# Kernel optimization log

Hardware: AMD Instinct MI355X
Metric: run time of the kernel (lower is better)

Reference implementation:

```python
import jax, jax.numpy as jnp
import numpy as np

B, N, T, D, H = 4, 8, 512, 256, 8
DK = D // H


def _dwconv(x, w, b=None):
    # x: (BN, D, T) depthwise conv, kernel 3, padding 'same', groups=D
    y = jax.lax.conv_general_dilated(
        x, w, window_strides=(1,), padding='SAME',
        feature_group_count=x.shape[1],
        dimension_numbers=('NCH', 'OIH', 'NCH'))
    if b is not None:
        y = y + b[None, :, None]
    return y


def setup_inputs() -> dict:
    key = jax.random.key(0)
    ks = jax.random.split(key, 16)
    s = 1.0 / np.sqrt(D)
    s3 = 1.0 / np.sqrt(3 * D)
    inp = {
        'query': jax.random.normal(ks[0], (B, N, T, D), jnp.float32),
        'key': jax.random.normal(ks[1], (B, N, T, D), jnp.float32),
        'value': jax.random.normal(ks[2], (B, N, T, D), jnp.float32),
        'key_padding_mask': jax.random.randint(ks[3], (B, N, T), 0, 2, jnp.int32),
        # depthwise conv params
        'w_pos': jax.random.uniform(ks[4], (D, 1, 3), jnp.float32, -0.577, 0.577),
        'b_pos': jax.random.uniform(ks[5], (D,), jnp.float32, -0.577, 0.577),
        # physics-initialized differential operators (still learnable floats)
        'w_vel': jnp.tile(jnp.array([-1.0, 0.0, 1.0], jnp.float32)[None, None, :], (D, 1, 1)),
        'w_acc': jnp.tile(jnp.array([1.0, -2.0, 1.0], jnp.float32)[None, None, :], (D, 1, 1)),
        # fusion / projection linears (stored as (in, out))
        'Wq': jax.random.uniform(ks[6], (3 * D, D), jnp.float32, -s3, s3),
        'bq': jax.random.uniform(ks[7], (D,), jnp.float32, -s3, s3),
        'Wk': jax.random.uniform(ks[8], (3 * D, D), jnp.float32, -s3, s3),
        'bk': jax.random.uniform(ks[9], (D,), jnp.float32, -s3, s3),
        'Wv': jax.random.uniform(ks[10], (D, D), jnp.float32, -s, s),
        'bv': jax.random.uniform(ks[11], (D,), jnp.float32, -s, s),
        'Wo': jax.random.uniform(ks[12], (D, D), jnp.float32, -s, s),
        'bo': jax.random.uniform(ks[13], (D,), jnp.float32, -s, s),
    }
    return inp


def reference(query, key, value, key_padding_mask,
              w_pos, b_pos, w_vel, w_acc,
              Wq, bq, Wk, bk, Wv, bv, Wo, bo):
    b, n, t, d = query.shape
    scale = jnp.float32(1.0 / np.sqrt(DK))

    def kin_feats(x):
        xin = x.reshape(b * n, t, d).transpose(0, 2, 1)  # (BN, D, T)
        p = _dwconv(xin, w_pos, b_pos)
        v = _dwconv(xin, w_vel)
        a = _dwconv(xin, w_acc)
        return jnp.concatenate([p, v, a], axis=1).transpose(0, 2, 1)  # (BN, T, 3D)

    qc = kin_feats(query)
    kc = kin_feats(key)

    Q = (qc @ Wq + bq).reshape(b, n, t, H, DK).transpose(0, 1, 3, 2, 4)  # (B,N,H,Tq,dk)
    K = (kc @ Wk + bk).reshape(b, n, t, H, DK).transpose(0, 1, 3, 2, 4)
    V = (value @ Wv + bv).reshape(b, n, t, H, DK).transpose(0, 1, 3, 2, 4)

    scores = jnp.einsum('bnhqd,bnhkd->bnhqk', Q, K) * scale
    mask = key_padding_mask.astype(bool)[:, :, None, None, :]  # (B,N,1,1,Tk)
    scores = jnp.where(mask, jnp.float32(-1e9), scores)
    attn = jax.nn.softmax(scores, axis=-1)  # dropout is identity in eval

    ctx = jnp.einsum('bnhqk,bnhkd->bnhqd', attn, V)
    ctx = ctx.transpose(0, 1, 3, 2, 4).reshape(b, n, t, d)
    return ctx @ Wo + bo
```

## Files before the change

kernel.cpp:

```cpp
#include <hip/hip_runtime.h>
#include <math.h>


typedef __attribute__((ext_vector_type(8))) short bf16x8;
typedef __attribute__((ext_vector_type(4))) float f32x4;
typedef __attribute__((ext_vector_type(16))) float f32x16;
typedef __attribute__((ext_vector_type(4))) int i32x4;

__device__ __forceinline__ unsigned short f2bf(float f) {
    unsigned u = __float_as_uint(f);
    return (unsigned short)((u + 0x7fff + ((u >> 16) & 1)) >> 16);
}
__device__ __forceinline__ float bf2f(unsigned short h) {
    return __uint_as_float(((unsigned)h) << 16);
}
__device__ __forceinline__ float ex2(float x) {
    float r; asm("v_exp_f32 %0, %1" : "=v"(r) : "v"(x)); return r;
}
__device__ __forceinline__ int cvtpk(float lo, float hi) {
    int r; asm("v_cvt_pk_bf16_f32 %0, %1, %2" : "=v"(r) : "v"(lo), "v"(hi)); return r;
}
__device__ __forceinline__ void gll16(const void* gsrc, const void* ldst) {
    __builtin_amdgcn_global_load_lds(
        (const __attribute__((address_space(1))) unsigned int*)gsrc,
        (__attribute__((address_space(3))) unsigned int*)ldst, 16, 0, 0);
}

#define SCL (0.17677669529663689f * 1.4426950408889634f)

#define OFF_ZERO 0u
#define OFF_BTQ  25231360u
#define OFF_BTK  25624576u
#define OFF_BEFF 26017792u
#define OFF_WVT  26019840u
#define OFF_WOT  26150912u
#define OFF_QB   26413056u
#define OFF_KB   34801664u
#define OFF_VV   43190272u
#define OFF_CTX  51578880u

__global__ __launch_bounds__(256) void prep(
    const float* __restrict__ Wq, const float* __restrict__ Wk,
    const float* __restrict__ bq, const float* __restrict__ bk,
    const float* __restrict__ wp, const float* __restrict__ wv,
    const float* __restrict__ wa, const float* __restrict__ b_pos,
    const float* __restrict__ Wv, const float* __restrict__ Wo,
    unsigned short* __restrict__ BtQ, unsigned short* __restrict__ BtK,
    float* __restrict__ beff, unsigned short* __restrict__ WVT,
    unsigned short* __restrict__ WOT, float* __restrict__ zeropage)
{
    int bid = blockIdx.x;
    if (bid < 1536) {
        int idx = bid * 256 + threadIdx.x;
        int which = idx / 196608;
        int r = idx - which * 196608;
        int j = r >> 16;
        int rem = r & 65535;
        int n = rem >> 8;
        int d = rem & 255;
        const float* W = which ? Wk : Wq;
        float val = wp[d * 3 + j] * W[d * 256 + n]
                  + wv[d * 3 + j] * W[(256 + d) * 256 + n]
                  + wa[d * 3 + j] * W[(512 + d) * 256 + n];
        if (!which) val *= SCL;
        (which ? BtK : BtQ)[n * 768 + j * 256 + d] = f2bf(val);
    } else if (bid < 2048) {
        int idx = (bid - 1536) * 256 + threadIdx.x;
        int which = idx >> 16;
        int r = idx & 65535;
        int n = r >> 8, kk = r & 255;
        if (!which) WVT[n * 256 + kk] = f2bf(Wv[kk * 256 + n]);
        else        WOT[n * 256 + kk] = f2bf(Wo[kk * 256 + n]);
    } else if (bid < 2050) {
        int which = bid - 2048;
        int n = threadIdx.x;
        const float* W = which ? Wk : Wq;
        const float* bb = which ? bk : bq;
        float s = bb[n];
        for (int d = 0; d < 256; ++d) s = fmaf(b_pos[d], W[d * 256 + n], s);
        if (!which) s *= SCL;
        beff[which * 256 + n] = s;
    } else {
        if (threadIdx.x < 64) zeropage[threadIdx.x] = 0.f;
    }
}

template<int KTOT, bool IM2COL>
__device__ __forceinline__ void gemmf32(
    const float* __restrict__ A, const unsigned short* __restrict__ Bt,
    const float* __restrict__ bias, const float* __restrict__ zeropage,
    unsigned short* __restrict__ Out, float* Asf, unsigned short* Bs)
{
    const int tid = threadIdx.x;
    const int wid = tid >> 6, l = tid & 63;
    const int l31 = l & 31, h2 = l >> 5;
    const int wm = wid >> 1, wn = wid & 1;
    const int m0 = blockIdx.x * 128, n0 = blockIdx.y * 128;

    f32x16 acc[2][2] = {};

    for (int k0 = 0; k0 < KTOT; k0 += 64) {
        __syncthreads();
        #pragma unroll
        for (int q = 0; q < 8; ++q) {
            int cidx = q * 256 + tid;
            int row = cidx >> 4, cch = cidx & 15;
            int csrc = (cch ^ (row & 15)) * 4;
            const float* asrc;
            if constexpr (IM2COL) {
                int seq = m0 >> 9, t0 = m0 & 511;
                int st = t0 + row + (k0 >> 8) - 1;
                asrc = (st >= 0 && st < 512)
                     ? A + ((size_t)(seq * 512 + st) * 256 + (k0 & 255) + csrc)
                     : zeropage + csrc;
            } else {
                asrc = A + ((size_t)(m0 + row) * 256 + k0 + csrc);
            }
            gll16(asrc, Asf + (size_t)cidx * 4);
        }
        #pragma unroll
        for (int q = 0; q < 4; ++q) {
            int cidx = q * 256 + tid;
            int row = cidx >> 3, c = cidx & 7;
            gll16(Bt + (size_t)(n0 + row) * KTOT + k0 + ((c ^ (row & 7)) * 8),
                  Bs + cidx * 8);
        }
        __syncthreads();
        #pragma unroll
        for (int ks = 0; ks < 4; ++ks) {
            const int c = ks * 2 + h2;
            bf16x8 af[2], bfr[2];
            #pragma unroll
            for (int mt = 0; mt < 2; ++mt) {
                int r = wm * 64 + mt * 32 + l31;
                f32x4 f0 = *(const f32x4*)&Asf[r * 64 + (((2 * c) ^ (r & 15)) * 4)];
                f32x4 f1 = *(const f32x4*)&Asf[r * 64 + (((2 * c + 1) ^ (r & 15)) * 4)];
                i32x4 w = {cvtpk(f0[0], f0[1]), cvtpk(f0[2], f0[3]),
                           cvtpk(f1[0], f1[1]), cvtpk(f1[2], f1[3])};
                af[mt] = __builtin_bit_cast(bf16x8, w);
            }
            #pragma unroll
            for (int nt = 0; nt < 2; ++nt) {
                int rn = wn * 64 + nt * 32 + l31;
                bfr[nt] = *(const bf16x8*)&Bs[rn * 64 + ((c ^ (rn & 7)) * 8)];
            }
            #pragma unroll
            for (int mt = 0; mt < 2; ++mt)
                #pragma unroll
                for (int nt = 0; nt < 2; ++nt)
                    acc[mt][nt] = __builtin_amdgcn_mfma_f32_32x32x16_bf16(af[mt], bfr[nt], acc[mt][nt], 0, 0, 0);
        }
    }

    #pragma unroll
    for (int nt = 0; nt < 2; ++nt) {
        const int col = n0 + wn * 64 + nt * 32 + l31;
        const float bb = bias[col];
        #pragma unroll
        for (int mt = 0; mt < 2; ++mt) {
            #pragma unroll
            for (int r = 0; r < 16; ++r) {
                const int row = m0 + wm * 64 + mt * 32 + 4 * h2 + (r & 3) + 8 * (r >> 2);
                Out[(size_t)row * 256 + col] = f2bf(acc[mt][nt][r] + bb);
            }
        }
    }
}

template<int KTOT, typename OutT>
__device__ __forceinline__ void gemm97(
    const unsigned short* __restrict__ A, const unsigned short* __restrict__ Bt,
    const float* __restrict__ bias, OutT* __restrict__ Out,
    unsigned short* As, unsigned short* Bs)
{
    const int tid = threadIdx.x;
    const int wid = tid >> 6, l = tid & 63;
    const int l31 = l & 31, h2 = l >> 5;
    const int wm = wid >> 1, wn = wid & 1;
    const int m0 = blockIdx.x * 128, n0 = blockIdx.y * 128;

    f32x16 acc[2][2] = {};

    for (int k0 = 0; k0 < KTOT; k0 += 64) {
        __syncthreads();
        #pragma unroll
        for (int q = 0; q < 4; ++q) {
            int cidx = q * 256 + tid;
            int row = cidx >> 3;
            int csrc = ((cidx & 7) ^ (row & 7)) * 8;
            gll16(A + (size_t)(m0 + row) * 256 + (k0 & 255) + csrc, As + (size_t)cidx * 8);
            gll16(Bt + (size_t)(n0 + row) * KTOT + k0 + csrc, Bs + (size_t)cidx * 8);
        }
        __syncthreads();
        #pragma unroll
        for (int ks = 0; ks < 4; ++ks) {
            bf16x8 af[2], bfr[2];
            #pragma unroll
            for (int mt = 0; mt < 2; ++mt) {
                int r = wm * 64 + mt * 32 + l31;
                af[mt] = *(const bf16x8*)&As[r * 64 + (((ks * 2 + h2) ^ (r & 7)) * 8)];
            }
            #pragma unroll
            for (int nt = 0; nt < 2; ++nt) {
                int rn = wn * 64 + nt * 32 + l31;
                bfr[nt] = *(const bf16x8*)&Bs[rn * 64 + (((ks * 2 + h2) ^ (rn & 7)) * 8)];
            }
            #pragma unroll
            for (int mt = 0; mt < 2; ++mt)
                #pragma unroll
                for (int nt = 0; nt < 2; ++nt)
                    acc[mt][nt] = __builtin_amdgcn_mfma_f32_32x32x16_bf16(af[mt], bfr[nt], acc[mt][nt], 0, 0, 0);
        }
    }

    #pragma unroll
    for (int nt = 0; nt < 2; ++nt) {
        const int col = n0 + wn * 64 + nt * 32 + l31;
        const float bb = bias[col];
        #pragma unroll
        for (int mt = 0; mt < 2; ++mt) {
            #pragma unroll
            for (int r = 0; r < 16; ++r) {
                const int row = m0 + wm * 64 + mt * 32 + 4 * h2 + (r & 3) + 8 * (r >> 2);
                float v = acc[mt][nt][r] + bb;
                if constexpr (sizeof(OutT) == 2) Out[(size_t)row * 256 + col] = (OutT)f2bf(v);
                else Out[(size_t)row * 256 + col] = v;
            }
        }
    }
}

__global__ __launch_bounds__(256) void proj_fused(
    const float* __restrict__ query, const float* __restrict__ key,
    const float* __restrict__ value,
    const unsigned short* __restrict__ BTQ, const unsigned short* __restrict__ BTK,
    const unsigned short* __restrict__ WVT,
    const float* __restrict__ BEFF, const float* __restrict__ bv,
    const float* __restrict__ zeropage,
    unsigned short* __restrict__ QB, unsigned short* __restrict__ KB,
    unsigned short* __restrict__ VV)
{
    __shared__ alignas(16) float Asf[8192];
    __shared__ alignas(16) unsigned short Bs[8192];
    const int z = blockIdx.z;
    if (z == 0)      gemmf32<768, true>(query, BTQ, BEFF, zeropage, QB, Asf, Bs);
    else if (z == 1) gemmf32<768, true>(key, BTK, BEFF + 256, zeropage, KB, Asf, Bs);
    else             gemmf32<256, false>(value, WVT, bv, zeropage, VV, Asf, Bs);
}

__global__ __launch_bounds__(256) void outproj(
    const unsigned short* __restrict__ CTX, const unsigned short* __restrict__ WOT,
    const float* __restrict__ bo, float* __restrict__ Out)
{
    __shared__ alignas(16) unsigned short As[8192];
    __shared__ alignas(16) unsigned short Bs[8192];
    gemm97<256, float>(CTX, WOT, bo, Out, As, Bs);
}

__global__ __launch_bounds__(512) void attn_mfma(const unsigned short* __restrict__ Qb,
                                                 const unsigned short* __restrict__ Kb,
                                                 const unsigned short* __restrict__ Vv,
                                                 const int* __restrict__ mask,
                                                 unsigned short* __restrict__ ctx) {
    __shared__ alignas(16) unsigned short Qs[512 * 32];
    __shared__ alignas(16) unsigned short Ks[2][128 * 32];
    __shared__ alignas(16) unsigned short VsT[2][32 * 136];
    __shared__ float Mb[2][128];

    const int bnh = blockIdx.x;
    const int bn = bnh >> 3, h = bnh & 7;
    const int tid = threadIdx.x, wid = tid >> 6, l = tid & 63;
    const int g = l >> 4, r15 = l & 15;
    const unsigned short* Qg = Qb + (size_t)bn * 512 * 256 + h * 32;
    const unsigned short* Kg = Kb + (size_t)bn * 512 * 256 + h * 32;
    const unsigned short* Vg = Vv + (size_t)bn * 512 * 256 + h * 32;
    const int* mp = mask + bn * 512;
    const int srow = tid >> 2;
    const int vkey = tid & 127, vd0 = (tid >> 7) * 8;

    auto stageK = [&](int k0, int b) {
        int csrc = (((tid & 3) ^ (srow & 3))) * 8;
        gll16(Kg + ((size_t)(k0 + srow)) * 256 + csrc, &Ks[b][wid * 512]);
    };

    #pragma unroll
    for (int q = 0; q < 4; ++q) {
        int chunk = q * 512 + tid;
        int row = chunk >> 2, c = chunk & 3;
        gll16(Qg + (size_t)row * 256 + c * 8, Qs + (q * 512 + wid * 64) * 8);
    }
    stageK(0, 0);
    {
        i32x4 vr = *(const i32x4*)(const void*)(Vg + (size_t)vkey * 256 + vd0);
        #pragma unroll
        for (int i = 0; i < 4; ++i) {
            unsigned u = (unsigned)vr[i];
            VsT[0][(vd0 + 2 * i) * 136 + vkey] = (unsigned short)(u & 0xffff);
            VsT[0][(vd0 + 2 * i + 1) * 136 + vkey] = (unsigned short)(u >> 16);
        }
        if (tid < 128) Mb[0][tid] = (mp[tid] != 0) ? -1e9f : 0.f;
    }
    __syncthreads();

    bf16x8 bq[4];
    #pragma unroll
    for (int qt = 0; qt < 4; ++qt)
        bq[qt] = *(const bf16x8*)&Qs[(qt * 128 + wid * 16 + r15) * 32 + g * 8];

    float mrun[4], lrun[4];
    f32x4 accO[4][2] = {};
    #pragma unroll
    for (int qt = 0; qt < 4; ++qt) { mrun[qt] = -1e30f; lrun[qt] = 0.f; }

    for (int kt = 0; kt < 4; ++kt) {
        const int cur = kt & 1, nxt = cur ^ 1;
        const int k0n = kt * 128 + 128;

        i32x4 vr;
        int mraw = 0;
        if (kt < 3) {
            stageK(k0n, nxt);
            vr = *(const i32x4*)(const void*)(Vg + ((size_t)(k0n + vkey)) * 256 + vd0);
            if (tid < 128) mraw = mp[k0n + tid];
        }

        bf16x8 av[2][4];
        #pragma unroll
        for (int mt = 0; mt < 2; ++mt)
            #pragma unroll
            for (int s = 0; s < 4; ++s)
                av[mt][s] = *(const bf16x8*)&VsT[cur][(mt * 16 + r15) * 136 + 32 * s + 8 * g];

        #pragma unroll
        for (int qt = 0; qt < 4; ++qt) {
            float p[8][4];
            float rmax = -3e38f;
            __builtin_amdgcn_s_setprio(1);
            #pragma unroll
            for (int t2 = 0; t2 < 8; ++t2) {
                const int base = 32 * (t2 >> 1) + 4 * (t2 & 1);
                const int arow = base + 8 * (r15 >> 2) + (r15 & 3);
                bf16x8 ak = *(const bf16x8*)&Ks[cur][arow * 32 + ((g ^ (arow & 3)) * 8)];
                f32x4 cin = *(const f32x4*)&Mb[cur][base + 8 * g];
                f32x4 st = __builtin_amdgcn_mfma_f32_16x16x32_bf16(ak, bq[qt], cin, 0, 0, 0);
                #pragma unroll
                for (int r = 0; r < 4; ++r) p[t2][r] = st[r];
                rmax = fmaxf(rmax, fmaxf(fmaxf(st[0], st[1]), fmaxf(st[2], st[3])));
            }
            __builtin_amdgcn_s_setprio(0);
            rmax = fmaxf(rmax, __shfl_xor(rmax, 16, 64));
            rmax = fmaxf(rmax, __shfl_xor(rmax, 32, 64));

            if (__ballot(rmax > mrun[qt])) {
                float mnew = fmaxf(mrun[qt], rmax);
                float fs = ex2(mrun[qt] - mnew);
                lrun[qt] *= fs;
                accO[qt][0] *= fs;
                accO[qt][1] *= fs;
                mrun[qt] = mnew;
            }
            float psum = 0.f;
            #pragma unroll
            for (int t2 = 0; t2 < 8; ++t2)
                #pragma unroll
                for (int r = 0; r < 4; ++r) {
                    float e = ex2(p[t2][r] - mrun[qt]);
                    p[t2][r] = e;
                    psum += e;
                }
            psum += __shfl_xor(psum, 16, 64);
            psum += __shfl_xor(psum, 32, 64);
            lrun[qt] += psum;

            bf16x8 pb[4];
            #pragma unroll
            for (int s = 0; s < 4; ++s) {
                i32x4 bi = {cvtpk(p[2 * s][0], p[2 * s][1]), cvtpk(p[2 * s][2], p[2 * s][3]),
                            cvtpk(p[2 * s + 1][0], p[2 * s + 1][1]), cvtpk(p[2 * s + 1][2], p[2 * s + 1][3])};
                pb[s] = __builtin_bit_cast(bf16x8, bi);
            }

            __builtin_amdgcn_s_setprio(1);
            #pragma unroll
            for (int mt = 0; mt < 2; ++mt)
                #pragma unroll
                for (int s = 0; s < 4; ++s)
                    accO[qt][mt] = __builtin_amdgcn_mfma_f32_16x16x32_bf16(av[mt][s], pb[s], accO[qt][mt], 0, 0, 0);
            __builtin_amdgcn_s_setprio(0);
        }

        if (kt < 3) {
            #pragma unroll
            for (int i = 0; i < 4; ++i) {
                unsigned u = (unsigned)vr[i];
                VsT[nxt][(vd0 + 2 * i) * 136 + vkey] = (unsigned short)(u & 0xffff);
                VsT[nxt][(vd0 + 2 * i + 1) * 136 + vkey] = (unsigned short)(u >> 16);
            }
            if (tid < 128) Mb[nxt][tid] = (mraw != 0) ? -1e9f : 0.f;
        }
        __syncthreads();
    }

    #pragma unroll
    for (int qt = 0; qt < 4; ++qt) {
        const float inv = 1.f / lrun[qt];
        const size_t orow = (size_t)bn * 512 + qt * 128 + wid * 16 + r15;
        #pragma unroll
        for (int mt = 0; mt < 2; ++mt) {
            ushort4 o;
            o.x = f2bf(accO[qt][mt][0] * inv);
            o.y = f2bf(accO[qt][mt][1] * inv);
            o.z = f2bf(accO[qt][mt][2] * inv);
            o.w = f2bf(accO[qt][mt][3] * inv);
            *(ushort4*)&ctx[orow * 256 + h * 32 + mt * 16 + 4 * g] = o;
        }
    }
}

extern "C" void kernel_launch(void* const* d_in, const int* in_sizes, int n_in,
                              void* d_out, int out_size, void* d_ws, size_t ws_size,
                              hipStream_t stream) {
    const float* query = (const float*)d_in[0];
    const float* key   = (const float*)d_in[1];
    const float* value = (const float*)d_in[2];
    const int*   kpm   = (const int*)d_in[3];
    const float* w_pos = (const float*)d_in[4];
    const float* b_pos = (const float*)d_in[5];
    const float* w_vel = (const float*)d_in[6];
    const float* w_acc = (const float*)d_in[7];
    const float* Wq    = (const float*)d_in[8];
    const float* bq    = (const float*)d_in[9];
    const float* Wk    = (const float*)d_in[10];
    const float* bk    = (const float*)d_in[11];
    const float* Wv    = (const float*)d_in[12];
    const float* bv    = (const float*)d_in[13];
    const float* Wo    = (const float*)d_in[14];
    const float* bo    = (const float*)d_in[15];

    unsigned char* w = (unsigned char*)d_ws;
    float*          ZP  = (float*)(w + OFF_ZERO);
    unsigned short* BTQ = (unsigned short*)(w + OFF_BTQ);
    unsigned short* BTK = (unsigned short*)(w + OFF_BTK);
    float*          BEFF= (float*)(w + OFF_BEFF);
    unsigned short* WVT = (unsigned short*)(w + OFF_WVT);
    unsigned short* WOT = (unsigned short*)(w + OFF_WOT);
    unsigned short* QB  = (unsigned short*)(w + OFF_QB);
    unsigned short* KB  = (unsigned short*)(w + OFF_KB);
    unsigned short* VV  = (unsigned short*)(w + OFF_VV);
    unsigned short* CTX = (unsigned short*)(w + OFF_CTX);

    prep<<<2051, 256, 0, stream>>>(Wq, Wk, bq, bk, w_pos, w_vel, w_acc, b_pos,
                                   Wv, Wo, BTQ, BTK, BEFF, WVT, WOT, ZP);

    proj_fused<<<dim3(128, 2, 3), 256, 0, stream>>>(query, key, value, BTQ, BTK, WVT,
                                                    BEFF, bv, ZP, QB, KB, VV);

    attn_mfma<<<256, 512, 0, stream>>>(QB, KB, VV, kpm, CTX);

    outproj<<<dim3(128, 2), 256, 0, stream>>>(CTX, WOT, bo, (float*)d_out);
}
```

Before: 80.77 us.

## Retile fp32 projection GEMM to 64x256 tiles so A is read once

The projection GEMM moves from 128x128 output tiles (two N-blocks per M-block) to 64-row by full-256-column tiles. The fp32 activations, including the im2col-shifted reads, are then loaded and converted to bf16 only once instead of twice, which cuts global A traffic and the repeated conversion work. In exchange the bf16 weight tile per k-step doubles. Each wave now holds four accumulators and does one A conversion per k-slice. The grid keeps the same block count, 256x1x3.

```diff
diff --git a/kernel.cpp b/kernel.cpp
--- a/kernel.cpp
+++ b/kernel.cpp
@@ -10,9 +10,6 @@
 __device__ __forceinline__ unsigned short f2bf(float f) {
     unsigned u = __float_as_uint(f);
     return (unsigned short)((u + 0x7fff + ((u >> 16) & 1)) >> 16);
-}
-__device__ __forceinline__ float bf2f(unsigned short h) {
-    return __uint_as_float(((unsigned)h) << 16);
 }
 __device__ __forceinline__ float ex2(float x) {
     float r; asm("v_exp_f32 %0, %1" : "=v"(r) : "v"(x)); return r;
@@ -95,14 +92,14 @@
     const int wid = tid >> 6, l = tid & 63;
     const int l31 = l & 31, h2 = l >> 5;
     const int wm = wid >> 1, wn = wid & 1;
-    const int m0 = blockIdx.x * 128, n0 = blockIdx.y * 128;
-
-    f32x16 acc[2][2] = {};
+    const int m0 = blockIdx.x * 64;
+
+    f32x16 acc[4] = {};
 
     for (int k0 = 0; k0 < KTOT; k0 += 64) {
         __syncthreads();
         #pragma unroll
-        for (int q = 0; q < 8; ++q) {
+        for (int q = 0; q < 4; ++q) {
             int cidx = q * 256 + tid;
             int row = cidx >> 4, cch = cidx & 15;
             int csrc = (cch ^ (row & 15)) * 4;
@@ -119,50 +116,39 @@
             gll16(asrc, Asf + (size_t)cidx * 4);
         }
         #pragma unroll
-        for (int q = 0; q < 4; ++q) {
+        for (int q = 0; q < 8; ++q) {
             int cidx = q * 256 + tid;
             int row = cidx >> 3, c = cidx & 7;
-            gll16(Bt + (size_t)(n0 + row) * KTOT + k0 + ((c ^ (row & 7)) * 8),
-                  Bs + cidx * 8);
+            gll16(Bt + (size_t)row * KTOT + k0 + ((c ^ (row & 7)) * 8),
+                  Bs + (size_t)cidx * 8);
         }
         __syncthreads();
         #pragma unroll
         for (int ks = 0; ks < 4; ++ks) {
             const int c = ks * 2 + h2;
-            bf16x8 af[2], bfr[2];
-            #pragma unroll
-            for (int mt = 0; mt < 2; ++mt) {
-                int r = wm * 64 + mt * 32 + l31;
-                f32x4 f0 = *(const f32x4*)&Asf[r * 64 + (((2 * c) ^ (r & 15)) * 4)];
-                f32x4 f1 = *(const f32x4*)&Asf[r * 64 + (((2 * c + 1) ^ (r & 15)) * 4)];
-                i32x4 w = {cvtpk(f0[0], f0[1]), cvtpk(f0[2], f0[3]),
-                           cvtpk(f1[0], f1[1]), cvtpk(f1[2], f1[3])};
-                af[mt] = __builtin_bit_cast(bf16x8, w);
-            }
-            #pragma unroll
-            for (int nt = 0; nt < 2; ++nt) {
-                int rn = wn * 64 + nt * 32 + l31;
-                bfr[nt] = *(const bf16x8*)&Bs[rn * 64 + ((c ^ (rn & 7)) * 8)];
-            }
-            #pragma unroll
-            for (int mt = 0; mt < 2; ++mt)
-                #pragma unroll
-                for (int nt = 0; nt < 2; ++nt)
-                    acc[mt][nt] = __builtin_amdgcn_mfma_f32_32x32x16_bf16(af[mt], bfr[nt], acc[mt][nt], 0, 0, 0);
-        }
-    }
-
-    #pragma unroll
-    for (int nt = 0; nt < 2; ++nt) {
-        const int col = n0 + wn * 64 + nt * 32 + l31;
+            const int r = wm * 32 + l31;
+            f32x4 f0 = *(const f32x4*)&Asf[r * 64 + (((2 * c) ^ (r & 15)) * 4)];
+            f32x4 f1 = *(const f32x4*)&Asf[r * 64 + (((2 * c + 1) ^ (r & 15)) * 4)];
+            i32x4 w = {cvtpk(f0[0], f0[1]), cvtpk(f0[2], f0[3]),
+                       cvtpk(f1[0], f1[1]), cvtpk(f1[2], f1[3])};
+            bf16x8 af = __builtin_bit_cast(bf16x8, w);
+            #pragma unroll
+            for (int nt = 0; nt < 4; ++nt) {
+                int rn = wn * 128 + nt * 32 + l31;
+                bf16x8 bfr = *(const bf16x8*)&Bs[rn * 64 + ((c ^ (rn & 7)) * 8)];
+                acc[nt] = __builtin_amdgcn_mfma_f32_32x32x16_bf16(af, bfr, acc[nt], 0, 0, 0);
+            }
+        }
+    }
+
+    #pragma unroll
+    for (int nt = 0; nt < 4; ++nt) {
+        const int col = wn * 128 + nt * 32 + l31;
         const float bb = bias[col];
         #pragma unroll
-        for (int mt = 0; mt < 2; ++mt) {
-            #pragma unroll
-            for (int r = 0; r < 16; ++r) {
-                const int row = m0 + wm * 64 + mt * 32 + 4 * h2 + (r & 3) + 8 * (r >> 2);
-                Out[(size_t)row * 256 + col] = f2bf(acc[mt][nt][r] + bb);
-            }
+        for (int r = 0; r < 16; ++r) {
+            const int row = m0 + wm * 32 + 4 * h2 + (r & 3) + 8 * (r >> 2);
+            Out[(size_t)row * 256 + col] = f2bf(acc[nt][r] + bb);
         }
     }
 }
@@ -240,8 +226,8 @@
     unsigned short* __restrict__ QB, unsigned short* __restrict__ KB,
     unsigned short* __restrict__ VV)
 {
-    __shared__ alignas(16) float Asf[8192];
-    __shared__ alignas(16) unsigned short Bs[8192];
+    __shared__ alignas(16) float Asf[4096];
+    __shared__ alignas(16) unsigned short Bs[16384];
     const int z = blockIdx.z;
     if (z == 0)      gemmf32<768, true>(query, BTQ, BEFF, zeropage, QB, Asf, Bs);
     else if (z == 1) gemmf32<768, true>(key, BTK, BEFF + 256, zeropage, KB, Asf, Bs);
@@ -452,7 +438,7 @@
     prep<<<2051, 256, 0, stream>>>(Wq, Wk, bq, bk, w_pos, w_vel, w_acc, b_pos,
                                    Wv, Wo, BTQ, BTK, BEFF, WVT, WOT, ZP);
 
-    proj_fused<<<dim3(128, 2, 3), 256, 0, stream>>>(query, key, value, BTQ, BTK, WVT,
+    proj_fused<<<dim3(256, 1, 3), 256, 0, stream>>>(query, key, value, BTQ, BTK, WVT,
                                                     BEFF, bv, ZP, QB, KB, VV);
 
     attn_mfma<<<256, 512, 0, stream>>>(QB, KB, VV, kpm, CTX);
```

Result: slower. 82.40 us (+2.0%).
